# Kernel tuning notes

Measured on AMD Instinct MI355X. Metric: run time of the kernel, lower is better.

## Reference

```python
import jax, jax.numpy as jnp
import numpy as np
import math

N, L, C, H, K = 4, 16384, 256, 8, 4
D = C // H


def setup_inputs():
    rng = jax.random.key(0)
    ks = jax.random.split(rng, 16)
    def w(k, shape, scale):
        return jax.random.normal(k, shape, jnp.float32) * scale
    s = 1.0 / math.sqrt(C)
    return {
        "query": jax.random.normal(ks[0], (N, L, C), jnp.float32),
        "key": jax.random.normal(ks[1], (N, L, C), jnp.float32),
        "value": jax.random.normal(ks[2], (N, L, C), jnp.float32),
        "reference_points": jax.random.uniform(ks[3], (N, L, 2), jnp.float32),
        "pos_embed": jax.random.normal(ks[4], (N, L, C), jnp.float32),
        "Wq": w(ks[5], (C, C), s), "bq": jnp.zeros((C,), jnp.float32),
        "Wk": w(ks[6], (C, C), s), "bk": jnp.zeros((C,), jnp.float32),
        "Wv": w(ks[7], (C, C), s), "bv": jnp.zeros((C,), jnp.float32),
        "Wo1": w(ks[8], (C, 2 * C), s), "bo1": jnp.zeros((2 * C,), jnp.float32),
        "Wo2": w(ks[9], (2 * C, H * K * 2), 0.02), "bo2": w(ks[10], (H * K * 2,), 0.02),
        "Wpos": w(ks[11], (C, C), s), "bpos": jnp.zeros((C,), jnp.float32),
        "Wout": w(ks[12], (C, C), s), "bout": jnp.zeros((C,), jnp.float32),
    }


def _sample_weight(points):
    # F.grid_sample on a 1x1 feature map (bilinear, zeros padding, align_corners=False)
    # degenerates to a scalar weight: grid g = 2p-1, unnormalized c = g/2 = p - 0.5,
    # pixel-0 bilinear weight per axis = max(0, 1 - |c|).
    c = points - 0.5
    return jax.nn.relu(1.0 - jnp.abs(c[..., 0])) * jax.nn.relu(1.0 - jnp.abs(c[..., 1]))


def reference(query, key, value, reference_points, pos_embed,
              Wq, bq, Wk, bk, Wv, bv, Wo1, bo1, Wo2, bo2, Wpos, bpos, Wout, bout):
    Nb, Ln, Cd = query.shape
    q = (query @ Wq + bq).reshape(Nb, Ln, H, D)
    k = (key @ Wk + bk).reshape(Nb, Ln, H, D)
    v = (value @ Wv + bv).reshape(Nb, Ln, H, D)
    pos = (pos_embed @ Wpos + bpos).reshape(Nb, Ln, H, D)
    q = q + pos
    k = k + pos
    # offset MLP: Linear(C,2C) -> ReLU -> Linear(2C, H*K*2)
    offsets = (jax.nn.relu(query @ Wo1 + bo1) @ Wo2 + bo2).reshape(Nb, Ln, H, K, 2)
    sp = reference_points[:, :, None, None, :] + offsets  # [N,L,H,K,2]
    w = _sample_weight(sp)                                # [N,L,H,K]
    # sampled_k[n,l,h,k,:] = k[n,l,h,:] * w[n,l,h,k]  (1x1 grid_sample closed form)
    qk = jnp.einsum('nlhd,nlhd->nlh', q, k)               # [N,L,H]
    attn = jax.nn.softmax(qk[..., None] * w / math.sqrt(D), axis=-1)  # [N,L,H,K]
    # output = sum_k attn_k * (v * w_k) = v * sum_k(attn_k * w_k)
    wv = jnp.sum(attn * w, axis=-1)                       # [N,L,H]
    out = (v * wv[..., None]).reshape(Nb, Ln, Cd)
    return out @ Wout + bout
```

## Files before the change

### kernel.cpp

```cpp
#include <hip/hip_runtime.h>
#include <hip/hip_bf16.h>

typedef __bf16 bf16x8 __attribute__((ext_vector_type(8)));
typedef float f32x4 __attribute__((ext_vector_type(4)));
typedef float f32x2 __attribute__((ext_vector_type(2)));

#define MT 64
#define CC 256

__device__ __forceinline__ int swz(int r, int c) {
    return r * 512 + ((c * 2) ^ ((r & 7) << 4));
}

__device__ __forceinline__ bf16x8 ldB(const __bf16* __restrict__ WT, int nc, int KC, int kc,
                                      int laneoff) {
    return *(const bf16x8*)(WT + ((size_t)nc * KC + kc) * 512 + laneoff);
}

__device__ __forceinline__ void stream_tile(const float* __restrict__ src, int row0, int tid,
                                            __bf16* dst) {
#pragma unroll
    for (int i = 0; i < 8; ++i) {
        int f = i * 512 + tid;
        int r = f >> 6;
        int c = (f & 63) * 4;
        f32x4 v = __builtin_nontemporal_load((const f32x4*)(src + (size_t)(row0 + r) * CC + c));
        union { __bf16 h[4]; unsigned long long u; } uu;
        uu.h[0] = (__bf16)v[0]; uu.h[1] = (__bf16)v[1];
        uu.h[2] = (__bf16)v[2]; uu.h[3] = (__bf16)v[3];
        *(unsigned long long*)((char*)dst + swz(r, c)) = uu.u;
    }
}

__global__ void prep_all(const float* __restrict__ Wq, const float* __restrict__ Wk,
                         const float* __restrict__ Wpos, const float* __restrict__ Wo1,
                         const float* __restrict__ Wo2, const float* __restrict__ Wv,
                         const float* __restrict__ Wout, __bf16* __restrict__ ws)
{
    int i = blockIdx.x * 256 + threadIdx.x;
    if (i >= 557056) return;
    int j, K, N;
    const float* S0 = nullptr; const float* S1 = nullptr;
    if (i < 131072)      { j = i;          K = 512; N = 256; S0 = Wq;  S1 = Wpos; }
    else if (i < 262144) { j = i - 131072; K = 512; N = 256; S0 = Wk;  S1 = Wpos; }
    else if (i < 393216) { j = i - 262144; K = 256; N = 512; S0 = Wo1; }
    else if (i < 425984) { j = i - 393216; K = 512; N = 64;  S0 = Wo2; }
    else if (i < 491520) { j = i - 425984; K = 256; N = 256; S0 = Wv; }
    else                 { j = i - 491520; K = 256; N = 256; S0 = Wout; }
    int tile = j >> 9, r = j & 511;
    int lane = r >> 3, e = r & 7;
    int q4 = lane >> 4, r16 = lane & 15;
    int KC = K >> 5;
    int nc = tile / KC, kc = tile - nc * KC;
    int k = kc * 32 + q4 * 8 + e;
    int n = nc * 16 + r16;
    float v;
    if (S1 && k >= 256) v = S1[(size_t)(k - 256) * N + n];
    else                v = S0[(size_t)k * N + n];
    ws[i] = (__bf16)v;
}

extern "C" __global__ void __launch_bounds__(512, 2)
fused_ext_attn(const float* __restrict__ query, const float* __restrict__ key,
               const float* __restrict__ value, const float* __restrict__ refp,
               const float* __restrict__ pose,
               const __bf16* __restrict__ ws,
               const float* __restrict__ bq, const float* __restrict__ bk,
               const float* __restrict__ bv, const float* __restrict__ bpos,
               const float* __restrict__ bo1, const float* __restrict__ bo2,
               const float* __restrict__ bout,
               float* __restrict__ out)
{
    const __bf16* WTqp  = ws;
    const __bf16* WTkp  = ws + 131072;
    const __bf16* WTo1  = ws + 262144;
    const __bf16* WTo2  = ws + 393216;
    const __bf16* WTv   = ws + 425984;
    const __bf16* WTout = ws + 491520;

    __shared__ __attribute__((aligned(16))) __bf16 SA[MT * CC];
    __shared__ __attribute__((aligned(16))) __bf16 SX[MT * CC];
    __shared__ __attribute__((aligned(16))) char   SY[16384];

    __bf16* off_b = (__bf16*)SY;
    float*  qk_s  = (float*)(SY + 8192);
    float*  wv_s  = (float*)(SY + 10240);

    const int tid = threadIdx.x;
    const int lane = tid & 63;
    const int wid = tid >> 6;
    const int r16 = lane & 15;
    const int q4 = lane >> 4;
    const int laneoff = lane * 8;
    const int row0 = blockIdx.x * MT;

    stream_tile(query, row0, tid, SA);
    __syncthreads();

    f32x4 accO[4];
#pragma unroll
    for (int i = 0; i < 4; ++i) accO[i] = (f32x4){0.f, 0.f, 0.f, 0.f};
    for (int p = 0; p < 2; ++p) {
        f32x4 acc[4][2];
#pragma unroll
        for (int i = 0; i < 4; ++i)
#pragma unroll
            for (int j = 0; j < 2; ++j) acc[i][j] = (f32x4){0.f, 0.f, 0.f, 0.f};
#pragma unroll
        for (int ks = 0; ks < 8; ++ks) {
            int ak = ks * 32 + q4 * 8;
            bf16x8 a[4], b[2];
#pragma unroll
            for (int mf = 0; mf < 4; ++mf)
                a[mf] = *(const bf16x8*)((const char*)SA + swz(mf * 16 + r16, ak));
#pragma unroll
            for (int nf = 0; nf < 2; ++nf)
                b[nf] = ldB(WTo1, p * 16 + wid * 2 + nf, 8, ks, laneoff);
#pragma unroll
            for (int mf = 0; mf < 4; ++mf)
#pragma unroll
                for (int nf = 0; nf < 2; ++nf)
                    acc[mf][nf] = __builtin_amdgcn_mfma_f32_16x16x32_bf16(a[mf], b[nf], acc[mf][nf], 0, 0, 0);
        }
#pragma unroll
        for (int mf = 0; mf < 4; ++mf)
#pragma unroll
            for (int nf = 0; nf < 2; ++nf) {
                int col = wid * 32 + nf * 16 + r16;
                float bias = bo1[p * 256 + col];
#pragma unroll
                for (int r = 0; r < 4; ++r)
                    *(__bf16*)((char*)SX + swz(mf * 16 + q4 * 4 + r, col)) =
                        (__bf16)fmaxf(acc[mf][nf][r] + bias, 0.f);
            }
        __syncthreads();
        if (wid < 4) {
#pragma unroll
            for (int ks = 0; ks < 8; ++ks) {
                int ak = ks * 32 + q4 * 8;
                bf16x8 b = ldB(WTo2, wid, 16, p * 8 + ks, laneoff);
#pragma unroll
                for (int mf = 0; mf < 4; ++mf) {
                    bf16x8 a = *(const bf16x8*)((const char*)SX + swz(mf * 16 + r16, ak));
                    accO[mf] = __builtin_amdgcn_mfma_f32_16x16x32_bf16(a, b, accO[mf], 0, 0, 0);
                }
            }
            if (p == 1) {
                int col = wid * 16 + r16;
                float b2 = bo2[col];
#pragma unroll
                for (int mf = 0; mf < 4; ++mf)
#pragma unroll
                    for (int r = 0; r < 4; ++r)
                        off_b[(mf * 16 + q4 * 4 + r) * 64 + col] = (__bf16)(accO[mf][r] + b2);
            }
        }
        __syncthreads();
    }

    f32x4 qa[4][2];
#pragma unroll
    for (int i = 0; i < 4; ++i)
#pragma unroll
        for (int j = 0; j < 2; ++j) qa[i][j] = (f32x4){0.f, 0.f, 0.f, 0.f};
    stream_tile(pose, row0, tid, SX);
#pragma unroll
    for (int ks = 0; ks < 8; ++ks) {
        int ak = ks * 32 + q4 * 8;
        bf16x8 a[4], b[2];
#pragma unroll
        for (int mf = 0; mf < 4; ++mf)
            a[mf] = *(const bf16x8*)((const char*)SA + swz(mf * 16 + r16, ak));
#pragma unroll
        for (int nf = 0; nf < 2; ++nf)
            b[nf] = ldB(WTqp, wid * 2 + nf, 16, ks, laneoff);
#pragma unroll
        for (int mf = 0; mf < 4; ++mf)
#pragma unroll
            for (int nf = 0; nf < 2; ++nf)
                qa[mf][nf] = __builtin_amdgcn_mfma_f32_16x16x32_bf16(a[mf], b[nf], qa[mf][nf], 0, 0, 0);
    }
    __syncthreads();

    stream_tile(key, row0, tid, SA);
#pragma unroll
    for (int ks = 8; ks < 16; ++ks) {
        int ak = (ks - 8) * 32 + q4 * 8;
        bf16x8 a[4], b[2];
#pragma unroll
        for (int mf = 0; mf < 4; ++mf)
            a[mf] = *(const bf16x8*)((const char*)SX + swz(mf * 16 + r16, ak));
#pragma unroll
        for (int nf = 0; nf < 2; ++nf)
            b[nf] = ldB(WTqp, wid * 2 + nf, 16, ks, laneoff);
#pragma unroll
        for (int mf = 0; mf < 4; ++mf)
#pragma unroll
            for (int nf = 0; nf < 2; ++nf)
                qa[mf][nf] = __builtin_amdgcn_mfma_f32_16x16x32_bf16(a[mf], b[nf], qa[mf][nf], 0, 0, 0);
    }
    __syncthreads();

    {
        f32x4 ka[4][2];
#pragma unroll
        for (int i = 0; i < 4; ++i)
#pragma unroll
            for (int j = 0; j < 2; ++j) ka[i][j] = (f32x4){0.f, 0.f, 0.f, 0.f};
#pragma unroll
        for (int ks = 0; ks < 16; ++ks) {
            int ak = (ks & 7) * 32 + q4 * 8;
            const char* Abase = (ks < 8) ? (const char*)SA : (const char*)SX;
            bf16x8 a[4], b[2];
#pragma unroll
            for (int mf = 0; mf < 4; ++mf)
                a[mf] = *(const bf16x8*)(Abase + swz(mf * 16 + r16, ak));
#pragma unroll
            for (int nf = 0; nf < 2; ++nf)
                b[nf] = ldB(WTkp, wid * 2 + nf, 16, ks, laneoff);
#pragma unroll
            for (int mf = 0; mf < 4; ++mf)
#pragma unroll
                for (int nf = 0; nf < 2; ++nf)
                    ka[mf][nf] = __builtin_amdgcn_mfma_f32_16x16x32_bf16(a[mf], b[nf], ka[mf][nf], 0, 0, 0);
        }
        float Bq[2], Bk[2];
#pragma unroll
        for (int nf = 0; nf < 2; ++nf) {
            int col = wid * 32 + nf * 16 + r16;
            Bq[nf] = bq[col] + bpos[col];
            Bk[nf] = bk[col] + bpos[col];
        }
#pragma unroll
        for (int mf = 0; mf < 4; ++mf)
#pragma unroll
            for (int r = 0; r < 4; ++r) {
                float p0 = (qa[mf][0][r] + Bq[0]) * (ka[mf][0][r] + Bk[0])
                         + (qa[mf][1][r] + Bq[1]) * (ka[mf][1][r] + Bk[1]);
#pragma unroll
                for (int m = 1; m < 16; m <<= 1)
                    p0 += __shfl_xor(p0, m);
                if (r16 == 0)
                    qk_s[(mf * 16 + q4 * 4 + r) * 8 + wid] = p0;
            }
    }
    __syncthreads();

    stream_tile(value, row0, tid, SA);
    {
        int t = tid >> 3, h = tid & 7;
        float qk = qk_s[t * 8 + h];
        f32x2 rp = __builtin_nontemporal_load((const f32x2*)(refp + (size_t)(row0 + t) * 2));
        float wgt[4], lg[4];
        float m = -1e30f;
#pragma unroll
        for (int kk = 0; kk < 4; ++kk) {
            float ox = (float)off_b[t * 64 + (h * 4 + kk) * 2];
            float oy = (float)off_b[t * 64 + (h * 4 + kk) * 2 + 1];
            float cx = rp[0] + ox - 0.5f, cy = rp[1] + oy - 0.5f;
            float wx = fmaxf(0.f, 1.f - fabsf(cx));
            float wy = fmaxf(0.f, 1.f - fabsf(cy));
            wgt[kk] = wx * wy;
            lg[kk] = qk * wgt[kk] * 0.17677669529663687f;
            m = fmaxf(m, lg[kk]);
        }
        float s = 0.f, sw = 0.f;
#pragma unroll
        for (int kk = 0; kk < 4; ++kk) {
            float e = __expf(lg[kk] - m);
            s += e;
            sw += e * wgt[kk];
        }
        wv_s[t * 8 + h] = sw / s;
    }
    __syncthreads();

    {
        f32x4 acc[4][2];
#pragma unroll
        for (int i = 0; i < 4; ++i)
#pragma unroll
            for (int j = 0; j < 2; ++j) acc[i][j] = (f32x4){0.f, 0.f, 0.f, 0.f};
#pragma unroll
        for (int ks = 0; ks < 8; ++ks) {
            int ak = ks * 32 + q4 * 8;
            bf16x8 a[4], b[2];
#pragma unroll
            for (int mf = 0; mf < 4; ++mf)
                a[mf] = *(const bf16x8*)((const char*)SA + swz(mf * 16 + r16, ak));
#pragma unroll
            for (int nf = 0; nf < 2; ++nf)
                b[nf] = ldB(WTv, wid * 2 + nf, 8, ks, laneoff);
#pragma unroll
            for (int mf = 0; mf < 4; ++mf)
#pragma unroll
                for (int nf = 0; nf < 2; ++nf)
                    acc[mf][nf] = __builtin_amdgcn_mfma_f32_16x16x32_bf16(a[mf], b[nf], acc[mf][nf], 0, 0, 0);
        }
#pragma unroll
        for (int mf = 0; mf < 4; ++mf)
#pragma unroll
            for (int nf = 0; nf < 2; ++nf) {
                int col = wid * 32 + nf * 16 + r16;
                float bias = bv[col];
#pragma unroll
                for (int r = 0; r < 4; ++r) {
                    int row = mf * 16 + q4 * 4 + r;
                    float wvv = wv_s[row * 8 + wid];
                    *(__bf16*)((char*)SX + swz(row, col)) = (__bf16)((acc[mf][nf][r] + bias) * wvv);
                }
            }
    }
    __syncthreads();

    {
        f32x4 acc[4][2];
#pragma unroll
        for (int i = 0; i < 4; ++i)
#pragma unroll
            for (int j = 0; j < 2; ++j) acc[i][j] = (f32x4){0.f, 0.f, 0.f, 0.f};
#pragma unroll
        for (int ks = 0; ks < 8; ++ks) {
            int ak = ks * 32 + q4 * 8;
            bf16x8 a[4], b[2];
#pragma unroll
            for (int mf = 0; mf < 4; ++mf)
                a[mf] = *(const bf16x8*)((const char*)SX + swz(mf * 16 + r16, ak));
#pragma unroll
            for (int nf = 0; nf < 2; ++nf)
                b[nf] = ldB(WTout, wid * 2 + nf, 8, ks, laneoff);
#pragma unroll
            for (int mf = 0; mf < 4; ++mf)
#pragma unroll
                for (int nf = 0; nf < 2; ++nf)
                    acc[mf][nf] = __builtin_amdgcn_mfma_f32_16x16x32_bf16(a[mf], b[nf], acc[mf][nf], 0, 0, 0);
        }
#pragma unroll
        for (int mf = 0; mf < 4; ++mf)
#pragma unroll
            for (int nf = 0; nf < 2; ++nf) {
                int col = wid * 32 + nf * 16 + r16;
                float bias = bout[col];
#pragma unroll
                for (int r = 0; r < 4; ++r) {
                    int row = mf * 16 + q4 * 4 + r;
                    __builtin_nontemporal_store(acc[mf][nf][r] + bias,
                                                out + (size_t)(row0 + row) * CC + col);
                }
            }
    }
}

extern "C" void kernel_launch(void* const* d_in, const int* in_sizes, int n_in,
                              void* d_out, int out_size, void* d_ws, size_t ws_size,
                              hipStream_t stream)
{
    const float* query = (const float*)d_in[0];
    const float* key   = (const float*)d_in[1];
    const float* value = (const float*)d_in[2];
    const float* refp  = (const float*)d_in[3];
    const float* pose  = (const float*)d_in[4];
    const float* Wq  = (const float*)d_in[5];  const float* bq   = (const float*)d_in[6];
    const float* Wk  = (const float*)d_in[7];  const float* bk   = (const float*)d_in[8];
    const float* Wv  = (const float*)d_in[9];  const float* bv   = (const float*)d_in[10];
    const float* Wo1 = (const float*)d_in[11]; const float* bo1  = (const float*)d_in[12];
    const float* Wo2 = (const float*)d_in[13]; const float* bo2  = (const float*)d_in[14];
    const float* Wpos= (const float*)d_in[15]; const float* bpos = (const float*)d_in[16];
    const float* Wout= (const float*)d_in[17]; const float* bout = (const float*)d_in[18];

    __bf16* ws = (__bf16*)d_ws;

    prep_all<<<2176, 256, 0, stream>>>(Wq, Wk, Wpos, Wo1, Wo2, Wv, Wout, ws);

    fused_ext_attn<<<65536 / MT, 512, 0, stream>>>(
        query, key, value, refp, pose, ws,
        bq, bk, bv, bpos, bo1, bo2, bout, (float*)d_out);
}
```

Measured before the change: 138.6 us.

## Double row tile to 128 and prefetch next input tile into registers during GEMMs

The row tile grows from 64 to 128 rows per block, so each weight fragment loaded from global memory is reused across twice as many rows. Input tiles (pose, key, value) are now loaded into registers before the preceding GEMM runs and written to shared memory afterwards, overlapping global loads with MFMA work. The Q projection is merged into a single 16-step loop, and all 8 waves now share the offset-MLP second layer. In exchange, shared memory per block roughly doubles and register pressure rises sharply (larger accumulators plus 16 prefetch registers). Launch bounds drop to one block per CU, halving occupancy and risking spills.

```diff
diff --git a/kernel.cpp b/kernel.cpp
--- a/kernel.cpp
+++ b/kernel.cpp
@@ -5,7 +5,7 @@
 typedef float f32x4 __attribute__((ext_vector_type(4)));
 typedef float f32x2 __attribute__((ext_vector_type(2)));
 
-#define MT 64
+#define MT 128
 #define CC 256
 
 __device__ __forceinline__ int swz(int r, int c) {
@@ -17,18 +17,28 @@
     return *(const bf16x8*)(WT + ((size_t)nc * KC + kc) * 512 + laneoff);
 }
 
-__device__ __forceinline__ void stream_tile(const float* __restrict__ src, int row0, int tid,
-                                            __bf16* dst) {
-#pragma unroll
-    for (int i = 0; i < 8; ++i) {
+__device__ __forceinline__ void stage_issue(const float* __restrict__ src, int row0, int tid,
+                                            unsigned long long (&h)[16]) {
+#pragma unroll
+    for (int i = 0; i < 16; ++i) {
         int f = i * 512 + tid;
         int r = f >> 6;
         int c = (f & 63) * 4;
         f32x4 v = __builtin_nontemporal_load((const f32x4*)(src + (size_t)(row0 + r) * CC + c));
-        union { __bf16 h[4]; unsigned long long u; } uu;
-        uu.h[0] = (__bf16)v[0]; uu.h[1] = (__bf16)v[1];
-        uu.h[2] = (__bf16)v[2]; uu.h[3] = (__bf16)v[3];
-        *(unsigned long long*)((char*)dst + swz(r, c)) = uu.u;
+        union { __bf16 b[4]; unsigned long long u; } uu;
+        uu.b[0] = (__bf16)v[0]; uu.b[1] = (__bf16)v[1];
+        uu.b[2] = (__bf16)v[2]; uu.b[3] = (__bf16)v[3];
+        h[i] = uu.u;
+    }
+}
+__device__ __forceinline__ void stage_retire(__bf16* dst, int tid,
+                                             const unsigned long long (&h)[16]) {
+#pragma unroll
+    for (int i = 0; i < 16; ++i) {
+        int f = i * 512 + tid;
+        int r = f >> 6;
+        int c = (f & 63) * 4;
+        *(unsigned long long*)((char*)dst + swz(r, c)) = h[i];
     }
 }
 
@@ -60,7 +70,7 @@
     ws[i] = (__bf16)v;
 }
 
-extern "C" __global__ void __launch_bounds__(512, 2)
+extern "C" __global__ void __launch_bounds__(512, 1)
 fused_ext_attn(const float* __restrict__ query, const float* __restrict__ key,
                const float* __restrict__ value, const float* __restrict__ refp,
                const float* __restrict__ pose,
@@ -79,12 +89,12 @@
     const __bf16* WTout = ws + 491520;
 
     __shared__ __attribute__((aligned(16))) __bf16 SA[MT * CC];
-    __shared__ __attribute__((aligned(16))) __bf16 SX[MT * CC];
-    __shared__ __attribute__((aligned(16))) char   SY[16384];
+    __shared__ __attribute__((aligned(16))) __bf16 SB[MT * CC];
+    __shared__ __attribute__((aligned(16))) char   SY[24576];
 
     __bf16* off_b = (__bf16*)SY;
-    float*  qk_s  = (float*)(SY + 8192);
-    float*  wv_s  = (float*)(SY + 10240);
+    float*  qk_s  = (float*)(SY + 16384);
+    float*  wv_s  = (float*)(SY + 20480);
 
     const int tid = threadIdx.x;
     const int lane = tid & 63;
@@ -94,132 +104,130 @@
     const int laneoff = lane * 8;
     const int row0 = blockIdx.x * MT;
 
-    stream_tile(query, row0, tid, SA);
-    __syncthreads();
-
+    {
+        unsigned long long hq[16];
+        stage_issue(query, row0, tid, hq);
+        stage_retire(SA, tid, hq);
+    }
+    __syncthreads();
+
+    unsigned long long hpose[16];
+    stage_issue(pose, row0, tid, hpose);
     f32x4 accO[4];
 #pragma unroll
     for (int i = 0; i < 4; ++i) accO[i] = (f32x4){0.f, 0.f, 0.f, 0.f};
     for (int p = 0; p < 2; ++p) {
-        f32x4 acc[4][2];
-#pragma unroll
-        for (int i = 0; i < 4; ++i)
+        f32x4 acc[8][2];
+#pragma unroll
+        for (int i = 0; i < 8; ++i)
 #pragma unroll
             for (int j = 0; j < 2; ++j) acc[i][j] = (f32x4){0.f, 0.f, 0.f, 0.f};
 #pragma unroll
         for (int ks = 0; ks < 8; ++ks) {
             int ak = ks * 32 + q4 * 8;
-            bf16x8 a[4], b[2];
-#pragma unroll
-            for (int mf = 0; mf < 4; ++mf)
+            bf16x8 a[8], b[2];
+#pragma unroll
+            for (int mf = 0; mf < 8; ++mf)
                 a[mf] = *(const bf16x8*)((const char*)SA + swz(mf * 16 + r16, ak));
 #pragma unroll
             for (int nf = 0; nf < 2; ++nf)
                 b[nf] = ldB(WTo1, p * 16 + wid * 2 + nf, 8, ks, laneoff);
 #pragma unroll
-            for (int mf = 0; mf < 4; ++mf)
+            for (int mf = 0; mf < 8; ++mf)
 #pragma unroll
                 for (int nf = 0; nf < 2; ++nf)
                     acc[mf][nf] = __builtin_amdgcn_mfma_f32_16x16x32_bf16(a[mf], b[nf], acc[mf][nf], 0, 0, 0);
         }
 #pragma unroll
-        for (int mf = 0; mf < 4; ++mf)
+        for (int mf = 0; mf < 8; ++mf)
 #pragma unroll
             for (int nf = 0; nf < 2; ++nf) {
-                int col = wid * 32 + nf * 16 + r16;
-                float bias = bo1[p * 256 + col];
+                int lcol = wid * 32 + nf * 16 + r16;
+                float bias = bo1[p * 256 + lcol];
 #pragma unroll
                 for (int r = 0; r < 4; ++r)
-                    *(__bf16*)((char*)SX + swz(mf * 16 + q4 * 4 + r, col)) =
+                    *(__bf16*)((char*)SB + swz(mf * 16 + q4 * 4 + r, lcol)) =
                         (__bf16)fmaxf(acc[mf][nf][r] + bias, 0.f);
             }
         __syncthreads();
-        if (wid < 4) {
+        {
+            int rbase = (wid >> 2) * 64;
 #pragma unroll
             for (int ks = 0; ks < 8; ++ks) {
                 int ak = ks * 32 + q4 * 8;
-                bf16x8 b = ldB(WTo2, wid, 16, p * 8 + ks, laneoff);
+                bf16x8 b = ldB(WTo2, wid & 3, 16, p * 8 + ks, laneoff);
 #pragma unroll
                 for (int mf = 0; mf < 4; ++mf) {
-                    bf16x8 a = *(const bf16x8*)((const char*)SX + swz(mf * 16 + r16, ak));
+                    bf16x8 a = *(const bf16x8*)((const char*)SB + swz(rbase + mf * 16 + r16, ak));
                     accO[mf] = __builtin_amdgcn_mfma_f32_16x16x32_bf16(a, b, accO[mf], 0, 0, 0);
                 }
             }
             if (p == 1) {
-                int col = wid * 16 + r16;
+                int col = (wid & 3) * 16 + r16;
                 float b2 = bo2[col];
 #pragma unroll
                 for (int mf = 0; mf < 4; ++mf)
 #pragma unroll
                     for (int r = 0; r < 4; ++r)
-                        off_b[(mf * 16 + q4 * 4 + r) * 64 + col] = (__bf16)(accO[mf][r] + b2);
+                        off_b[(rbase + mf * 16 + q4 * 4 + r) * 64 + col] = (__bf16)(accO[mf][r] + b2);
             }
         }
         __syncthreads();
     }
 
-    f32x4 qa[4][2];
-#pragma unroll
-    for (int i = 0; i < 4; ++i)
+    stage_retire(SB, tid, hpose);
+    __syncthreads();
+
+    unsigned long long hkey[16];
+    stage_issue(key, row0, tid, hkey);
+    f32x4 qa[8][2];
+#pragma unroll
+    for (int i = 0; i < 8; ++i)
 #pragma unroll
         for (int j = 0; j < 2; ++j) qa[i][j] = (f32x4){0.f, 0.f, 0.f, 0.f};
-    stream_tile(pose, row0, tid, SX);
-#pragma unroll
-    for (int ks = 0; ks < 8; ++ks) {
-        int ak = ks * 32 + q4 * 8;
-        bf16x8 a[4], b[2];
-#pragma unroll
-        for (int mf = 0; mf < 4; ++mf)
-            a[mf] = *(const bf16x8*)((const char*)SA + swz(mf * 16 + r16, ak));
+#pragma unroll
+    for (int ks = 0; ks < 16; ++ks) {
+        int ak = (ks & 7) * 32 + q4 * 8;
+        const char* Abase = (ks < 8) ? (const char*)SA : (const char*)SB;
+        bf16x8 a[8], b[2];
+#pragma unroll
+        for (int mf = 0; mf < 8; ++mf)
+            a[mf] = *(const bf16x8*)(Abase + swz(mf * 16 + r16, ak));
 #pragma unroll
         for (int nf = 0; nf < 2; ++nf)
             b[nf] = ldB(WTqp, wid * 2 + nf, 16, ks, laneoff);
 #pragma unroll
-        for (int mf = 0; mf < 4; ++mf)
+        for (int mf = 0; mf < 8; ++mf)
 #pragma unroll
             for (int nf = 0; nf < 2; ++nf)
                 qa[mf][nf] = __builtin_amdgcn_mfma_f32_16x16x32_bf16(a[mf], b[nf], qa[mf][nf], 0, 0, 0);
     }
     __syncthreads();
 
-    stream_tile(key, row0, tid, SA);
-#pragma unroll
-    for (int ks = 8; ks < 16; ++ks) {
-        int ak = (ks - 8) * 32 + q4 * 8;
-        bf16x8 a[4], b[2];
-#pragma unroll
-        for (int mf = 0; mf < 4; ++mf)
-            a[mf] = *(const bf16x8*)((const char*)SX + swz(mf * 16 + r16, ak));
-#pragma unroll
-        for (int nf = 0; nf < 2; ++nf)
-            b[nf] = ldB(WTqp, wid * 2 + nf, 16, ks, laneoff);
-#pragma unroll
-        for (int mf = 0; mf < 4; ++mf)
-#pragma unroll
-            for (int nf = 0; nf < 2; ++nf)
-                qa[mf][nf] = __builtin_amdgcn_mfma_f32_16x16x32_bf16(a[mf], b[nf], qa[mf][nf], 0, 0, 0);
-    }
-    __syncthreads();
-
+    stage_retire(SA, tid, hkey);
+    __syncthreads();
+
+    unsigned long long hval[16];
+    stage_issue(value, row0, tid, hval);
     {
-        f32x4 ka[4][2];
-#pragma unroll
-        for (int i = 0; i < 4; ++i)
+        f32x4 ka[8][2];
+#pragma unroll
+        for (int i = 0; i < 8; ++i)
 #pragma unroll
             for (int j = 0; j < 2; ++j) ka[i][j] = (f32x4){0.f, 0.f, 0.f, 0.f};
 #pragma unroll
         for (int ks = 0; ks < 16; ++ks) {
             int ak = (ks & 7) * 32 + q4 * 8;
-            const char* Abase = (ks < 8) ? (const char*)SA : (const char*)SX;
-            bf16x8 a[4], b[2];
-#pragma unroll
-            for (int mf = 0; mf < 4; ++mf)
+            const char* Abase = (ks < 8) ? (const char*)SA : (const char*)SB;
+            bf16x8 a[8], b[2];
+#pragma unroll
+            for (int mf = 0; mf < 8; ++mf)
                 a[mf] = *(const bf16x8*)(Abase + swz(mf * 16 + r16, ak));
 #pragma unroll
             for (int nf = 0; nf < 2; ++nf)
                 b[nf] = ldB(WTkp, wid * 2 + nf, 16, ks, laneoff);
 #pragma unroll
-            for (int mf = 0; mf < 4; ++mf)
+            for (int mf = 0; mf < 8; ++mf)
 #pragma unroll
                 for (int nf = 0; nf < 2; ++nf)
                     ka[mf][nf] = __builtin_amdgcn_mfma_f32_16x16x32_bf16(a[mf], b[nf], ka[mf][nf], 0, 0, 0);
@@ -232,23 +240,25 @@
             Bk[nf] = bk[col] + bpos[col];
         }
 #pragma unroll
-        for (int mf = 0; mf < 4; ++mf)
+        for (int mf = 0; mf < 8; ++mf)
 #pragma unroll
             for (int r = 0; r < 4; ++r) {
-                float p0 = (qa[mf][0][r] + Bq[0]) * (ka[mf][0][r] + Bk[0])
-                         + (qa[mf][1][r] + Bq[1]) * (ka[mf][1][r] + Bk[1]);
+                float p = (qa[mf][0][r] + Bq[0]) * (ka[mf][0][r] + Bk[0])
+                        + (qa[mf][1][r] + Bq[1]) * (ka[mf][1][r] + Bk[1]);
 #pragma unroll
                 for (int m = 1; m < 16; m <<= 1)
-                    p0 += __shfl_xor(p0, m);
+                    p += __shfl_xor(p, m);
                 if (r16 == 0)
-                    qk_s[(mf * 16 + q4 * 4 + r) * 8 + wid] = p0;
-            }
-    }
-    __syncthreads();
-
-    stream_tile(value, row0, tid, SA);
-    {
-        int t = tid >> 3, h = tid & 7;
+                    qk_s[(mf * 16 + q4 * 4 + r) * 8 + wid] = p;
+            }
+    }
+    __syncthreads();
+
+    stage_retire(SA, tid, hval);
+#pragma unroll
+    for (int pi = 0; pi < 2; ++pi) {
+        int idx = tid + pi * 512;
+        int t = idx >> 3, h = idx & 7;
         float qk = qk_s[t * 8 + h];
         f32x2 rp = __builtin_nontemporal_load((const f32x2*)(refp + (size_t)(row0 + t) * 2));
         float wgt[4], lg[4];
@@ -276,29 +286,29 @@
     __syncthreads();
 
     {
-        f32x4 acc[4][2];
-#pragma unroll
-        for (int i = 0; i < 4; ++i)
+        f32x4 acc[8][2];
+#pragma unroll
+        for (int i = 0; i < 8; ++i)
 #pragma unroll
             for (int j = 0; j < 2; ++j) acc[i][j] = (f32x4){0.f, 0.f, 0.f, 0.f};
 #pragma unroll
         for (int ks = 0; ks < 8; ++ks) {
             int ak = ks * 32 + q4 * 8;
-            bf16x8 a[4], b[2];
-#pragma unroll
-            for (int mf = 0; mf < 4; ++mf)
+            bf16x8 a[8], b[2];
+#pragma unroll
+            for (int mf = 0; mf < 8; ++mf)
                 a[mf] = *(const bf16x8*)((const char*)SA + swz(mf * 16 + r16, ak));
 #pragma unroll
             for (int nf = 0; nf < 2; ++nf)
                 b[nf] = ldB(WTv, wid * 2 + nf, 8, ks, laneoff);
 #pragma unroll
-            for (int mf = 0; mf < 4; ++mf)
+            for (int mf = 0; mf < 8; ++mf)
 #pragma unroll
                 for (int nf = 0; nf < 2; ++nf)
                     acc[mf][nf] = __builtin_amdgcn_mfma_f32_16x16x32_bf16(a[mf], b[nf], acc[mf][nf], 0, 0, 0);
         }
 #pragma unroll
-        for (int mf = 0; mf < 4; ++mf)
+        for (int mf = 0; mf < 8; ++mf)
 #pragma unroll
             for (int nf = 0; nf < 2; ++nf) {
                 int col = wid * 32 + nf * 16 + r16;
@@ -307,36 +317,36 @@
                 for (int r = 0; r < 4; ++r) {
                     int row = mf * 16 + q4 * 4 + r;
                     float wvv = wv_s[row * 8 + wid];
-                    *(__bf16*)((char*)SX + swz(row, col)) = (__bf16)((acc[mf][nf][r] + bias) * wvv);
+                    *(__bf16*)((char*)SB + swz(row, col)) = (__bf16)((acc[mf][nf][r] + bias) * wvv);
                 }
             }
     }
     __syncthreads();
 
     {
-        f32x4 acc[4][2];
-#pragma unroll
-        for (int i = 0; i < 4; ++i)
+        f32x4 acc[8][2];
+#pragma unroll
+        for (int i = 0; i < 8; ++i)
 #pragma unroll
             for (int j = 0; j < 2; ++j) acc[i][j] = (f32x4){0.f, 0.f, 0.f, 0.f};
 #pragma unroll
         for (int ks = 0; ks < 8; ++ks) {
             int ak = ks * 32 + q4 * 8;
-            bf16x8 a[4], b[2];
-#pragma unroll
-            for (int mf = 0; mf < 4; ++mf)
-                a[mf] = *(const bf16x8*)((const char*)SX + swz(mf * 16 + r16, ak));
+            bf16x8 a[8], b[2];
+#pragma unroll
+            for (int mf = 0; mf < 8; ++mf)
+                a[mf] = *(const bf16x8*)((const char*)SB + swz(mf * 16 + r16, ak));
 #pragma unroll
             for (int nf = 0; nf < 2; ++nf)
                 b[nf] = ldB(WTout, wid * 2 + nf, 8, ks, laneoff);
 #pragma unroll
-            for (int mf = 0; mf < 4; ++mf)
+            for (int mf = 0; mf < 8; ++mf)
 #pragma unroll
                 for (int nf = 0; nf < 2; ++nf)
                     acc[mf][nf] = __builtin_amdgcn_mfma_f32_16x16x32_bf16(a[mf], b[nf], acc[mf][nf], 0, 0, 0);
         }
 #pragma unroll
-        for (int mf = 0; mf < 4; ++mf)
+        for (int mf = 0; mf < 8; ++mf)
 #pragma unroll
             for (int nf = 0; nf < 2; ++nf) {
                 int col = wid * 32 + nf * 16 + r16;
```

Result: slower. 236.6 us (+70.7%).
